# Kernel tuning notes

Measured on AMD Instinct MI355X. Metric: run time of the kernel, lower is better.

## Reference

```python
import jax, jax.numpy as jnp
import numpy as np

ALPHA = 0.2  # LeakyReLU negative slope
NEG_INF = -1e9


def setup_inputs() -> dict:
    key = jax.random.key(0)
    k1, k2, k3, k4 = jax.random.split(key, 4)
    B, N, IN, OUT = 8, 2048, 512, 32
    graph_input = jax.random.normal(k1, (B, N, IN), dtype=jnp.float32)
    adj = jax.random.randint(k2, (B, N, N), 0, 2, dtype=jnp.int32)
    W_fc = jax.random.normal(k3, (OUT, IN), dtype=jnp.float32) * (1.0 / np.sqrt(IN))
    W_attn = jax.random.normal(k4, (1, 2 * OUT), dtype=jnp.float32) * (1.0 / np.sqrt(2 * OUT))
    return {"graph_input": graph_input, "adj": adj, "W_fc": W_fc, "W_attn": W_attn}


def reference(graph_input, adj, W_fc, W_attn):
    # h: [B, N, 32]
    h = jnp.einsum('bni,oi->bno', graph_input, W_fc)
    out_dim = W_fc.shape[0]
    # attn_fc(cat(h_i, h_j)) is separable: a1.h_i + a2.h_j
    a1 = W_attn[0, :out_dim]   # [32]
    a2 = W_attn[0, out_dim:]   # [32]
    f1 = jnp.einsum('bno,o->bn', h, a1)  # [B, N]
    f2 = jnp.einsum('bno,o->bn', h, a2)  # [B, N]
    scores = jax.nn.leaky_relu(f1[:, :, None] + f2[:, None, :], negative_slope=ALPHA)  # [B,N,N]
    scores = jnp.where(adj == 0, NEG_INF, scores)
    attn = jax.nn.softmax(scores, axis=2)
    # NOTE: original multiplies attention with graph_input (not h)
    h_prime = jnp.einsum('bnm,bmi->bni', attn, graph_input)  # [B, N, IN]
    return jax.nn.elu(h_prime)  # concat=True path
```

## Files before the change

kernel.cpp:

```cpp
#include <hip/hip_runtime.h>
#include <hip/hip_bf16.h>

#define BATCH 8
#define NN    2048
#define FIN   512
#define FOUT  32
#define GALPHA 0.2f
#define NROW  128
#define NIT   32

typedef float  f32x4  __attribute__((ext_vector_type(4)));
typedef __bf16 bf16x8 __attribute__((ext_vector_type(8)));
typedef unsigned short u16;
typedef u16 u16x8 __attribute__((ext_vector_type(8)));

static __device__ __forceinline__ u16 f2bf(float f) {
    __hip_bfloat16 h = __float2bfloat16(f);
    union { __hip_bfloat16 h; u16 u; } c; c.h = h; return c.u;
}
static __device__ __forceinline__ float bf2f(u16 u) {
    union { u16 u; __hip_bfloat16 h; } c; c.u = u; return __bfloat162float(c.h);
}

__global__ __launch_bounds__(256) void k_prep(
    const float* __restrict__ x, const int* __restrict__ adj,
    const float* __restrict__ Wfc, const float* __restrict__ Wat,
    __hip_bfloat16* __restrict__ xt,
    float* __restrict__ f1, float* __restrict__ f2,
    unsigned int* __restrict__ bits)
{
    const int bx = blockIdx.x;
    const int it = bx & 7, mt = (bx >> 3) & 31, b = bx >> 8;
    const int m0 = mt * 64, i0 = it * 64;
    const int tt = threadIdx.x;

    __shared__ __align__(16) char smem[16384];
    u16 (*tile)[72]   = (u16(*)[72])smem;
    float* w1s        = (float*)(smem + 9216);
    float* w2s        = (float*)(smem + 9216 + 256);
    unsigned int* pls = (unsigned int*)smem;

    if (tt < 64) {
        const int i = i0 + tt;
        float s1 = 0.f, s2 = 0.f;
        #pragma unroll
        for (int o = 0; o < FOUT; o++) {
            float wv = Wfc[o * FIN + i];
            s1 += wv * Wat[o];
            s2 += wv * Wat[FOUT + o];
        }
        w1s[tt] = s1; w2s[tt] = s2;
    }
    __syncthreads();

    const int mm  = tt >> 3;
    const int icl = (tt & 7) * 8;
    const float* xb = x + ((size_t)b * NN + m0) * FIN + i0;
    f32x4 wA = *(const f32x4*)&w1s[icl];
    f32x4 wB = *(const f32x4*)&w1s[icl + 4];
    f32x4 wC = *(const f32x4*)&w2s[icl];
    f32x4 wD = *(const f32x4*)&w2s[icl + 4];
    float p1[2], p2[2];
    #pragma unroll
    for (int h = 0; h < 2; h++) {
        int m = mm + h * 32;
        const f32x4* src = (const f32x4*)(xb + (size_t)m * FIN + icl);
        f32x4 v0 = src[0], v1 = src[1];
        u16x8 pk;
        float s1 = 0.f, s2 = 0.f;
        #pragma unroll
        for (int j = 0; j < 4; j++) {
            pk[j] = f2bf(v0[j]); pk[4 + j] = f2bf(v1[j]);
            s1 += v0[j] * wA[j] + v1[j] * wB[j];
            s2 += v0[j] * wC[j] + v1[j] * wD[j];
        }
        p1[h] = s1; p2[h] = s2;
        *(u16x8*)&tile[m][icl] = pk;
    }
    #pragma unroll
    for (int off = 1; off < 8; off <<= 1) {
        p1[0] += __shfl_xor(p1[0], off); p1[1] += __shfl_xor(p1[1], off);
        p2[0] += __shfl_xor(p2[0], off); p2[1] += __shfl_xor(p2[1], off);
    }
    if ((tt & 7) == 0) {
        size_t r0 = (size_t)b * NN + m0 + mm;
        atomicAdd(&f1[r0], p1[0]);      atomicAdd(&f1[r0 + 32], p1[1]);
        atomicAdd(&f2[r0], p2[0]);      atomicAdd(&f2[r0 + 32], p2[1]);
    }
    __syncthreads();
    __hip_bfloat16* xtb = xt + ((size_t)b * FIN + i0) * NN + m0;
    const int mc = (tt & 7) * 8;
    #pragma unroll
    for (int h = 0; h < 2; h++) {
        int ii = (tt >> 3) + h * 32;
        u16x8 v;
        #pragma unroll
        for (int j = 0; j < 8; j++) v[j] = tile[mc + j][ii];
        *(u16x8*)(xtb + (size_t)ii * NN + mc) = v;
    }

    __syncthreads();
    {
        const int* ab = adj + (size_t)(b * NN + m0 + it * 8) * NN;
        #pragma unroll
        for (int s = 0; s < 16; s++) {
            int4 v = *(const int4*)(ab + (size_t)(s * 256 + tt) * 4);
            unsigned int pb = (v.x != 0 ? 0x00000001u : 0u)
                            | (v.y != 0 ? 0x00000100u : 0u)
                            | (v.z != 0 ? 0x00010000u : 0u)
                            | (v.w != 0 ? 0x01000000u : 0u);
            pls[s * 256 + tt] = pb;
        }
        __syncthreads();
        const int r = tt >> 5, c0 = tt & 31;
        #pragma unroll
        for (int half = 0; half < 2; half++) {
            const int c = c0 + half * 32;
            const unsigned int* q = pls + r * 512 + c * 8;
            unsigned int bv = 0;
            #pragma unroll
            for (int j = 0; j < 8; j++) {
                unsigned int pb = q[j];
                bv |= (pb         & 1u) << (j * 4 + 0);
                bv |= ((pb >> 8)  & 1u) << (j * 4 + 1);
                bv |= ((pb >> 16) & 1u) << (j * 4 + 2);
                bv |= ((pb >> 24) & 1u) << (j * 4 + 3);
            }
            bits[(size_t)(b * NN + m0 + it * 8 + r) * 64 + c] = bv;
        }
    }
}

__global__ __launch_bounds__(512, 2) void k_main(
    const unsigned int* __restrict__ bits, const __hip_bfloat16* __restrict__ xt,
    const float* __restrict__ f1, const float* __restrict__ f2,
    float* __restrict__ out)
{
    const int bx = blockIdx.x;
    const int b = bx & 7, rt = (bx >> 3) & 15, it = bx >> 7;
    const int n0 = rt * NROW;
    const int i0 = it * 256;
    const int tid = threadIdx.x;
    const int lane = tid & 63, wv = tid >> 6;
    const int quad = lane >> 4, l15 = lane & 15;

    __shared__ u16 At[2][NROW * 64];
    __shared__ float rs[NROW];

    const int grow = tid >> 2;
    const int q4   = tid & 3;
    const unsigned short* bp = (const unsigned short*)bits
                               + ((size_t)(b * NN) + n0 + grow) * 128 + q4;
    const float* f2p = f2 + b * NN + q4 * 16;
    const float  f1v = f1[b * NN + n0 + grow];
    const int swz = grow & 7;
    u16* wp0 = &At[0][grow * 64 + (((q4 * 2) ^ swz) * 8)];
    u16* wp1 = &At[0][grow * 64 + (((q4 * 2 + 1) ^ swz) * 8)];
    float rpart = 0.f;

    const __hip_bfloat16* xtp = xt + ((size_t)(b * FIN) + i0 + wv * 32 + l15) * NN + quad * 8;

    f32x4 acc[8][2];
    #pragma unroll
    for (int s = 0; s < 8; s++) { acc[s][0] = (f32x4){0,0,0,0}; acc[s][1] = (f32x4){0,0,0,0}; }

    auto gen = [&](int buf, unsigned int bv, const f32x4* fr) {
        u16x8 pk0, pk1;
        #pragma unroll
        for (int e = 0; e < 16; e++) {
            float s  = f1v + fr[e >> 2][e & 3];
            float ls = fmaxf(s, GALPHA * s);
            float ev = ((bv >> e) & 1u) ? __expf(ls) : 0.f;
            u16 hb = f2bf(ev);
            rpart += bf2f(hb);
            if (e < 8) pk0[e] = hb; else pk1[e - 8] = hb;
        }
        *(u16x8*)(wp0 + buf * (NROW * 64)) = pk0;
        *(u16x8*)(wp1 + buf * (NROW * 64)) = pk1;
    };

    {
        unsigned int b0 = bp[0];
        f32x4 g0[4];
        #pragma unroll
        for (int j = 0; j < 4; j++) g0[j] = *(const f32x4*)(f2p + j * 4);
        gen(0, b0, g0);
    }
    unsigned int brng[2];
    f32x4 frng[2][4];
    brng[1] = bp[4];
    #pragma unroll
    for (int j = 0; j < 4; j++) frng[1][j] = *(const f32x4*)(f2p + 64 + j * 4);
    brng[0] = bp[8];
    #pragma unroll
    for (int j = 0; j < 4; j++) frng[0][j] = *(const f32x4*)(f2p + 128 + j * 4);

    bf16x8 Bc[2][2], Bn[2][2];
    #pragma unroll
    for (int ks = 0; ks < 2; ks++)
        #pragma unroll
        for (int c = 0; c < 2; c++)
            Bc[ks][c] = *(const bf16x8*)(xtp + ks * 32 + (size_t)(c * 16) * NN);
    __syncthreads();

    #pragma unroll 2
    for (int t = 0; t < NIT; t++) {
        const int cur = t & 1;
        if (t < NIT - 1) {
            const __hip_bfloat16* xk = xtp + (t + 1) * 64;
            #pragma unroll
            for (int ks = 0; ks < 2; ks++)
                #pragma unroll
                for (int c = 0; c < 2; c++)
                    Bn[ks][c] = *(const bf16x8*)(xk + ks * 32 + (size_t)(c * 16) * NN);
        }
        #pragma unroll
        for (int ks = 0; ks < 2; ks++) {
            #pragma unroll
            for (int s = 0; s < 8; s++) {
                const int row = s * 16 + l15;
                bf16x8 Af = *(const bf16x8*)&At[cur][row * 64 + (((ks * 4 + quad) ^ (row & 7)) * 8)];
                acc[s][0] = __builtin_amdgcn_mfma_f32_16x16x32_bf16(Af, Bc[ks][0], acc[s][0], 0, 0, 0);
                acc[s][1] = __builtin_amdgcn_mfma_f32_16x16x32_bf16(Af, Bc[ks][1], acc[s][1], 0, 0, 0);
            }
        }
        if (t < NIT - 1) {
            gen(1 - cur, brng[(t + 1) & 1], frng[(t + 1) & 1]);
            if (t < NIT - 2) {
                brng[t & 1] = bp[(t + 2) * 4];
                #pragma unroll
                for (int j = 0; j < 4; j++)
                    frng[t & 1][j] = *(const f32x4*)(f2p + (t + 2) * 64 + j * 4);
            }
        }
        asm volatile("s_waitcnt lgkmcnt(0)\ns_barrier" ::: "memory");
        #pragma unroll
        for (int ks = 0; ks < 2; ks++) {
            Bc[ks][0] = Bn[ks][0]; Bc[ks][1] = Bn[ks][1];
        }
    }

    rpart += __shfl_xor(rpart, 1);
    rpart += __shfl_xor(rpart, 2);
    if (q4 == 0) rs[grow] = 1.0f / rpart;
    __syncthreads();

    #pragma unroll
    for (int s = 0; s < 8; s++) {
        #pragma unroll
        for (int r = 0; r < 4; r++) {
            const int row = s * 16 + quad * 4 + r;
            const float inv = rs[row];
            float* op = out + ((size_t)b * NN + (n0 + row)) * FIN + i0 + wv * 32 + l15;
            #pragma unroll
            for (int c = 0; c < 2; c++) {
                float v = acc[s][c][r] * inv;
                v = v > 0.f ? v : (__expf(v) - 1.f);
                op[c * 16] = v;
            }
        }
    }
}

extern "C" void kernel_launch(void* const* d_in, const int* in_sizes, int n_in,
                              void* d_out, int out_size, void* d_ws, size_t ws_size,
                              hipStream_t stream) {
    const float* x   = (const float*)d_in[0];
    const int*   adj = (const int*)d_in[1];
    const float* Wfc = (const float*)d_in[2];
    const float* Wat = (const float*)d_in[3];
    float* out = (float*)d_out;

    float* f1 = (float*)d_ws;
    float* f2 = f1 + BATCH * NN;
    unsigned int* bits = (unsigned int*)(f2 + BATCH * NN);
    __hip_bfloat16* xt = (__hip_bfloat16*)(bits + (size_t)BATCH * NN * 64);

    hipMemsetAsync(f1, 0, (size_t)2 * BATCH * NN * sizeof(float), stream);
    hipLaunchKernelGGL(k_prep, dim3(2048), dim3(256), 0, stream,
                       x, adj, Wfc, Wat, xt, f1, f2, bits);
    hipLaunchKernelGGL(k_main, dim3(256),  dim3(512), 0, stream,
                       bits, xt, f1, f2, out);
}
```

Measured before the change: 284.1 us.

## Fuse prep and main kernels into one cooperative launch with grid sync

Merges the preprocessing kernel (bf16 transpose of x, f1/f2 projection, adjacency bit-packing) and the attention-matmul kernel into a single cooperative kernel separated by a grid-wide barrier. Each prep block now owns a full 64-row strip across all 512 features, so f1/f2 are written directly instead of atomically accumulated, which removes the memset. This saves a launch and the memset but drops prep from 2048 blocks to 256 blocks looping serially. That may reduce memory-level parallelism in the bandwidth-bound adjacency read, and it adds grid-sync overhead.

```diff
diff --git a/kernel.cpp b/kernel.cpp
--- a/kernel.cpp
+++ b/kernel.cpp
@@ -1,5 +1,8 @@
 #include <hip/hip_runtime.h>
 #include <hip/hip_bf16.h>
+#include <hip/hip_cooperative_groups.h>
+
+namespace cg = cooperative_groups;
 
 #define BATCH 8
 #define NN    2048
@@ -22,241 +25,237 @@
     union { u16 u; __hip_bfloat16 h; } c; c.u = u; return __bfloat162float(c.h);
 }
 
-__global__ __launch_bounds__(256) void k_prep(
+__global__ __launch_bounds__(512, 2) void k_fused(
     const float* __restrict__ x, const int* __restrict__ adj,
     const float* __restrict__ Wfc, const float* __restrict__ Wat,
     __hip_bfloat16* __restrict__ xt,
     float* __restrict__ f1, float* __restrict__ f2,
-    unsigned int* __restrict__ bits)
-{
-    const int bx = blockIdx.x;
-    const int it = bx & 7, mt = (bx >> 3) & 31, b = bx >> 8;
-    const int m0 = mt * 64, i0 = it * 64;
-    const int tt = threadIdx.x;
-
-    __shared__ __align__(16) char smem[16384];
-    u16 (*tile)[72]   = (u16(*)[72])smem;
-    float* w1s        = (float*)(smem + 9216);
-    float* w2s        = (float*)(smem + 9216 + 256);
-    unsigned int* pls = (unsigned int*)smem;
-
-    if (tt < 64) {
-        const int i = i0 + tt;
-        float s1 = 0.f, s2 = 0.f;
-        #pragma unroll
-        for (int o = 0; o < FOUT; o++) {
-            float wv = Wfc[o * FIN + i];
-            s1 += wv * Wat[o];
-            s2 += wv * Wat[FOUT + o];
-        }
-        w1s[tt] = s1; w2s[tt] = s2;
-    }
-    __syncthreads();
-
-    const int mm  = tt >> 3;
-    const int icl = (tt & 7) * 8;
-    const float* xb = x + ((size_t)b * NN + m0) * FIN + i0;
-    f32x4 wA = *(const f32x4*)&w1s[icl];
-    f32x4 wB = *(const f32x4*)&w1s[icl + 4];
-    f32x4 wC = *(const f32x4*)&w2s[icl];
-    f32x4 wD = *(const f32x4*)&w2s[icl + 4];
-    float p1[2], p2[2];
-    #pragma unroll
-    for (int h = 0; h < 2; h++) {
-        int m = mm + h * 32;
-        const f32x4* src = (const f32x4*)(xb + (size_t)m * FIN + icl);
-        f32x4 v0 = src[0], v1 = src[1];
-        u16x8 pk;
-        float s1 = 0.f, s2 = 0.f;
-        #pragma unroll
-        for (int j = 0; j < 4; j++) {
-            pk[j] = f2bf(v0[j]); pk[4 + j] = f2bf(v1[j]);
-            s1 += v0[j] * wA[j] + v1[j] * wB[j];
-            s2 += v0[j] * wC[j] + v1[j] * wD[j];
-        }
-        p1[h] = s1; p2[h] = s2;
-        *(u16x8*)&tile[m][icl] = pk;
-    }
-    #pragma unroll
-    for (int off = 1; off < 8; off <<= 1) {
-        p1[0] += __shfl_xor(p1[0], off); p1[1] += __shfl_xor(p1[1], off);
-        p2[0] += __shfl_xor(p2[0], off); p2[1] += __shfl_xor(p2[1], off);
-    }
-    if ((tt & 7) == 0) {
-        size_t r0 = (size_t)b * NN + m0 + mm;
-        atomicAdd(&f1[r0], p1[0]);      atomicAdd(&f1[r0 + 32], p1[1]);
-        atomicAdd(&f2[r0], p2[0]);      atomicAdd(&f2[r0 + 32], p2[1]);
-    }
-    __syncthreads();
-    __hip_bfloat16* xtb = xt + ((size_t)b * FIN + i0) * NN + m0;
-    const int mc = (tt & 7) * 8;
-    #pragma unroll
-    for (int h = 0; h < 2; h++) {
-        int ii = (tt >> 3) + h * 32;
-        u16x8 v;
-        #pragma unroll
-        for (int j = 0; j < 8; j++) v[j] = tile[mc + j][ii];
-        *(u16x8*)(xtb + (size_t)ii * NN + mc) = v;
-    }
-
-    __syncthreads();
-    {
-        const int* ab = adj + (size_t)(b * NN + m0 + it * 8) * NN;
-        #pragma unroll
-        for (int s = 0; s < 16; s++) {
-            int4 v = *(const int4*)(ab + (size_t)(s * 256 + tt) * 4);
-            unsigned int pb = (v.x != 0 ? 0x00000001u : 0u)
-                            | (v.y != 0 ? 0x00000100u : 0u)
-                            | (v.z != 0 ? 0x00010000u : 0u)
-                            | (v.w != 0 ? 0x01000000u : 0u);
-            pls[s * 256 + tt] = pb;
-        }
-        __syncthreads();
-        const int r = tt >> 5, c0 = tt & 31;
-        #pragma unroll
-        for (int half = 0; half < 2; half++) {
-            const int c = c0 + half * 32;
-            const unsigned int* q = pls + r * 512 + c * 8;
-            unsigned int bv = 0;
-            #pragma unroll
-            for (int j = 0; j < 8; j++) {
-                unsigned int pb = q[j];
-                bv |= (pb         & 1u) << (j * 4 + 0);
-                bv |= ((pb >> 8)  & 1u) << (j * 4 + 1);
-                bv |= ((pb >> 16) & 1u) << (j * 4 + 2);
-                bv |= ((pb >> 24) & 1u) << (j * 4 + 3);
-            }
-            bits[(size_t)(b * NN + m0 + it * 8 + r) * 64 + c] = bv;
-        }
-    }
-}
-
-__global__ __launch_bounds__(512, 2) void k_main(
-    const unsigned int* __restrict__ bits, const __hip_bfloat16* __restrict__ xt,
-    const float* __restrict__ f1, const float* __restrict__ f2,
+    unsigned int* __restrict__ bits,
     float* __restrict__ out)
 {
-    const int bx = blockIdx.x;
-    const int b = bx & 7, rt = (bx >> 3) & 15, it = bx >> 7;
-    const int n0 = rt * NROW;
-    const int i0 = it * 256;
-    const int tid = threadIdx.x;
-    const int lane = tid & 63, wv = tid >> 6;
-    const int quad = lane >> 4, l15 = lane & 15;
-
-    __shared__ u16 At[2][NROW * 64];
-    __shared__ float rs[NROW];
-
-    const int grow = tid >> 2;
-    const int q4   = tid & 3;
-    const unsigned short* bp = (const unsigned short*)bits
-                               + ((size_t)(b * NN) + n0 + grow) * 128 + q4;
-    const float* f2p = f2 + b * NN + q4 * 16;
-    const float  f1v = f1[b * NN + n0 + grow];
-    const int swz = grow & 7;
-    u16* wp0 = &At[0][grow * 64 + (((q4 * 2) ^ swz) * 8)];
-    u16* wp1 = &At[0][grow * 64 + (((q4 * 2 + 1) ^ swz) * 8)];
-    float rpart = 0.f;
-
-    const __hip_bfloat16* xtp = xt + ((size_t)(b * FIN) + i0 + wv * 32 + l15) * NN + quad * 8;
-
-    f32x4 acc[8][2];
-    #pragma unroll
-    for (int s = 0; s < 8; s++) { acc[s][0] = (f32x4){0,0,0,0}; acc[s][1] = (f32x4){0,0,0,0}; }
-
-    auto gen = [&](int buf, unsigned int bv, const f32x4* fr) {
-        u16x8 pk0, pk1;
-        #pragma unroll
-        for (int e = 0; e < 16; e++) {
-            float s  = f1v + fr[e >> 2][e & 3];
-            float ls = fmaxf(s, GALPHA * s);
-            float ev = ((bv >> e) & 1u) ? __expf(ls) : 0.f;
-            u16 hb = f2bf(ev);
-            rpart += bf2f(hb);
-            if (e < 8) pk0[e] = hb; else pk1[e - 8] = hb;
-        }
-        *(u16x8*)(wp0 + buf * (NROW * 64)) = pk0;
-        *(u16x8*)(wp1 + buf * (NROW * 64)) = pk1;
-    };
+    __shared__ __align__(16) char smem[33280];
+    const int tt = threadIdx.x;
 
     {
-        unsigned int b0 = bp[0];
-        f32x4 g0[4];
-        #pragma unroll
-        for (int j = 0; j < 4; j++) g0[j] = *(const f32x4*)(f2p + j * 4);
-        gen(0, b0, g0);
+        const int b  = blockIdx.x >> 5;
+        const int mt = blockIdx.x & 31;
+        const int m0 = mt * 64;
+        u16 (*tile)[72]   = (u16(*)[72])smem;
+        float* w1s        = (float*)(smem + 9216);
+        float* w2s        = (float*)(smem + 11264);
+        unsigned int* pls = (unsigned int*)(smem + 13312);
+
+        {
+            float s1 = 0.f, s2 = 0.f;
+            #pragma unroll
+            for (int o = 0; o < FOUT; o++) {
+                float wv = Wfc[o * FIN + tt];
+                s1 += wv * Wat[o];
+                s2 += wv * Wat[FOUT + o];
+            }
+            w1s[tt] = s1; w2s[tt] = s2;
+        }
+        __syncthreads();
+
+        const int mm  = tt >> 3;
+        const int icl = (tt & 7) * 8;
+        float f1a = 0.f, f2a = 0.f;
+
+        for (int it = 0; it < 8; it++) {
+            const int i0 = it * 64;
+            const f32x4* src = (const f32x4*)(x + ((size_t)(b * NN + m0 + mm)) * FIN + i0 + icl);
+            f32x4 v0 = src[0], v1 = src[1];
+            f32x4 wA = *(const f32x4*)&w1s[i0 + icl];
+            f32x4 wB = *(const f32x4*)&w1s[i0 + icl + 4];
+            f32x4 wC = *(const f32x4*)&w2s[i0 + icl];
+            f32x4 wD = *(const f32x4*)&w2s[i0 + icl + 4];
+            u16x8 pk;
+            float s1 = 0.f, s2 = 0.f;
+            #pragma unroll
+            for (int j = 0; j < 4; j++) {
+                pk[j] = f2bf(v0[j]); pk[4 + j] = f2bf(v1[j]);
+                s1 += v0[j] * wA[j] + v1[j] * wB[j];
+                s2 += v0[j] * wC[j] + v1[j] * wD[j];
+            }
+            f1a += s1; f2a += s2;
+            *(u16x8*)&tile[mm][icl] = pk;
+            __syncthreads();
+            {
+                __hip_bfloat16* xtb = xt + ((size_t)b * FIN + i0) * NN + m0;
+                const int ii = tt >> 3;
+                const int mc = (tt & 7) * 8;
+                u16x8 v;
+                #pragma unroll
+                for (int j = 0; j < 8; j++) v[j] = tile[mc + j][ii];
+                *(u16x8*)(xtb + (size_t)ii * NN + mc) = v;
+            }
+            {
+                const int* ab = adj + (size_t)(b * NN + m0 + it * 8) * NN;
+                #pragma unroll
+                for (int s = 0; s < 8; s++) {
+                    int4 v = *(const int4*)(ab + (size_t)(s * 512 + tt) * 4);
+                    unsigned int pb = (v.x != 0 ? 0x00000001u : 0u)
+                                    | (v.y != 0 ? 0x00000100u : 0u)
+                                    | (v.z != 0 ? 0x00010000u : 0u)
+                                    | (v.w != 0 ? 0x01000000u : 0u);
+                    pls[s * 512 + tt] = pb;
+                }
+            }
+            __syncthreads();
+            {
+                const int r = tt >> 6, c = tt & 63;
+                const unsigned int* q = pls + r * 512 + c * 8;
+                unsigned int bv = 0;
+                #pragma unroll
+                for (int j = 0; j < 8; j++) {
+                    unsigned int pb = q[j];
+                    bv |= (pb         & 1u) << (j * 4 + 0);
+                    bv |= ((pb >> 8)  & 1u) << (j * 4 + 1);
+                    bv |= ((pb >> 16) & 1u) << (j * 4 + 2);
+                    bv |= ((pb >> 24) & 1u) << (j * 4 + 3);
+                }
+                bits[(size_t)(b * NN + m0 + it * 8 + r) * 64 + c] = bv;
+            }
+            if (it < 7) __syncthreads();
+        }
+        #pragma unroll
+        for (int off = 1; off < 8; off <<= 1) {
+            f1a += __shfl_xor(f1a, off);
+            f2a += __shfl_xor(f2a, off);
+        }
+        if ((tt & 7) == 0) {
+            f1[b * NN + m0 + mm] = f1a;
+            f2[b * NN + m0 + mm] = f2a;
+        }
     }
-    unsigned int brng[2];
-    f32x4 frng[2][4];
-    brng[1] = bp[4];
-    #pragma unroll
-    for (int j = 0; j < 4; j++) frng[1][j] = *(const f32x4*)(f2p + 64 + j * 4);
-    brng[0] = bp[8];
-    #pragma unroll
-    for (int j = 0; j < 4; j++) frng[0][j] = *(const f32x4*)(f2p + 128 + j * 4);
-
-    bf16x8 Bc[2][2], Bn[2][2];
-    #pragma unroll
-    for (int ks = 0; ks < 2; ks++)
-        #pragma unroll
-        for (int c = 0; c < 2; c++)
-            Bc[ks][c] = *(const bf16x8*)(xtp + ks * 32 + (size_t)(c * 16) * NN);
-    __syncthreads();
-
-    #pragma unroll 2
-    for (int t = 0; t < NIT; t++) {
-        const int cur = t & 1;
-        if (t < NIT - 1) {
-            const __hip_bfloat16* xk = xtp + (t + 1) * 64;
-            #pragma unroll
-            for (int ks = 0; ks < 2; ks++)
-                #pragma unroll
-                for (int c = 0; c < 2; c++)
-                    Bn[ks][c] = *(const bf16x8*)(xk + ks * 32 + (size_t)(c * 16) * NN);
-        }
-        #pragma unroll
-        for (int ks = 0; ks < 2; ks++) {
-            #pragma unroll
-            for (int s = 0; s < 8; s++) {
-                const int row = s * 16 + l15;
-                bf16x8 Af = *(const bf16x8*)&At[cur][row * 64 + (((ks * 4 + quad) ^ (row & 7)) * 8)];
-                acc[s][0] = __builtin_amdgcn_mfma_f32_16x16x32_bf16(Af, Bc[ks][0], acc[s][0], 0, 0, 0);
-                acc[s][1] = __builtin_amdgcn_mfma_f32_16x16x32_bf16(Af, Bc[ks][1], acc[s][1], 0, 0, 0);
-            }
-        }
-        if (t < NIT - 1) {
-            gen(1 - cur, brng[(t + 1) & 1], frng[(t + 1) & 1]);
-            if (t < NIT - 2) {
-                brng[t & 1] = bp[(t + 2) * 4];
-                #pragma unroll
-                for (int j = 0; j < 4; j++)
-                    frng[t & 1][j] = *(const f32x4*)(f2p + (t + 2) * 64 + j * 4);
-            }
-        }
-        asm volatile("s_waitcnt lgkmcnt(0)\ns_barrier" ::: "memory");
-        #pragma unroll
-        for (int ks = 0; ks < 2; ks++) {
-            Bc[ks][0] = Bn[ks][0]; Bc[ks][1] = Bn[ks][1];
-        }
-    }
-
-    rpart += __shfl_xor(rpart, 1);
-    rpart += __shfl_xor(rpart, 2);
-    if (q4 == 0) rs[grow] = 1.0f / rpart;
-    __syncthreads();
-
-    #pragma unroll
-    for (int s = 0; s < 8; s++) {
-        #pragma unroll
-        for (int r = 0; r < 4; r++) {
-            const int row = s * 16 + quad * 4 + r;
-            const float inv = rs[row];
-            float* op = out + ((size_t)b * NN + (n0 + row)) * FIN + i0 + wv * 32 + l15;
-            #pragma unroll
-            for (int c = 0; c < 2; c++) {
-                float v = acc[s][c][r] * inv;
-                v = v > 0.f ? v : (__expf(v) - 1.f);
-                op[c * 16] = v;
+
+    __threadfence();
+    cg::this_grid().sync();
+
+    {
+        const int bx = blockIdx.x;
+        const int b = bx & 7, rt = (bx >> 3) & 15, it = bx >> 7;
+        const int n0 = rt * NROW;
+        const int i0 = it * 256;
+        const int tid = tt;
+        const int lane = tid & 63, wv = tid >> 6;
+        const int quad = lane >> 4, l15 = lane & 15;
+
+        u16* Atb  = (u16*)smem;
+        float* rs = (float*)(smem + 32768);
+
+        const int grow = tid >> 2;
+        const int q4   = tid & 3;
+        const unsigned short* bp = (const unsigned short*)bits
+                                   + ((size_t)(b * NN) + n0 + grow) * 128 + q4;
+        const float* f2p = f2 + b * NN + q4 * 16;
+        const float  f1v = f1[b * NN + n0 + grow];
+        const int swz = grow & 7;
+        u16* wp0 = Atb + grow * 64 + (((q4 * 2) ^ swz) * 8);
+        u16* wp1 = Atb + grow * 64 + (((q4 * 2 + 1) ^ swz) * 8);
+        float rpart = 0.f;
+
+        const __hip_bfloat16* xtp = xt + ((size_t)(b * FIN) + i0 + wv * 32 + l15) * NN + quad * 8;
+
+        f32x4 acc[8][2];
+        #pragma unroll
+        for (int s = 0; s < 8; s++) { acc[s][0] = (f32x4){0,0,0,0}; acc[s][1] = (f32x4){0,0,0,0}; }
+
+        auto gen = [&](int buf, unsigned int bv, const f32x4* fr) {
+            u16x8 pk0, pk1;
+            #pragma unroll
+            for (int e = 0; e < 16; e++) {
+                float s  = f1v + fr[e >> 2][e & 3];
+                float ls = fmaxf(s, GALPHA * s);
+                float ev = ((bv >> e) & 1u) ? __expf(ls) : 0.f;
+                u16 hb = f2bf(ev);
+                rpart += bf2f(hb);
+                if (e < 8) pk0[e] = hb; else pk1[e - 8] = hb;
+            }
+            *(u16x8*)(wp0 + buf * (NROW * 64)) = pk0;
+            *(u16x8*)(wp1 + buf * (NROW * 64)) = pk1;
+        };
+
+        {
+            unsigned int b0 = bp[0];
+            f32x4 g0[4];
+            #pragma unroll
+            for (int j = 0; j < 4; j++) g0[j] = *(const f32x4*)(f2p + j * 4);
+            gen(0, b0, g0);
+        }
+        unsigned int brng[2];
+        f32x4 frng[2][4];
+        brng[1] = bp[4];
+        #pragma unroll
+        for (int j = 0; j < 4; j++) frng[1][j] = *(const f32x4*)(f2p + 64 + j * 4);
+        brng[0] = bp[8];
+        #pragma unroll
+        for (int j = 0; j < 4; j++) frng[0][j] = *(const f32x4*)(f2p + 128 + j * 4);
+
+        bf16x8 Bc[2][2], Bn[2][2];
+        #pragma unroll
+        for (int ks = 0; ks < 2; ks++)
+            #pragma unroll
+            for (int c = 0; c < 2; c++)
+                Bc[ks][c] = *(const bf16x8*)(xtp + ks * 32 + (size_t)(c * 16) * NN);
+        __syncthreads();
+
+        #pragma unroll 2
+        for (int t = 0; t < NIT; t++) {
+            const int cur = t & 1;
+            if (t < NIT - 1) {
+                const __hip_bfloat16* xk = xtp + (t + 1) * 64;
+                #pragma unroll
+                for (int ks = 0; ks < 2; ks++)
+                    #pragma unroll
+                    for (int c = 0; c < 2; c++)
+                        Bn[ks][c] = *(const bf16x8*)(xk + ks * 32 + (size_t)(c * 16) * NN);
+            }
+            #pragma unroll
+            for (int ks = 0; ks < 2; ks++) {
+                #pragma unroll
+                for (int s = 0; s < 8; s++) {
+                    const int row = s * 16 + l15;
+                    bf16x8 Af = *(const bf16x8*)(Atb + cur * (NROW * 64)
+                                  + row * 64 + (((ks * 4 + quad) ^ (row & 7)) * 8));
+                    acc[s][0] = __builtin_amdgcn_mfma_f32_16x16x32_bf16(Af, Bc[ks][0], acc[s][0], 0, 0, 0);
+                    acc[s][1] = __builtin_amdgcn_mfma_f32_16x16x32_bf16(Af, Bc[ks][1], acc[s][1], 0, 0, 0);
+                }
+            }
+            if (t < NIT - 1) {
+                gen(1 - cur, brng[(t + 1) & 1], frng[(t + 1) & 1]);
+                if (t < NIT - 2) {
+                    brng[t & 1] = bp[(t + 2) * 4];
+                    #pragma unroll
+                    for (int j = 0; j < 4; j++)
+                        frng[t & 1][j] = *(const f32x4*)(f2p + (t + 2) * 64 + j * 4);
+                }
+            }
+            asm volatile("s_waitcnt lgkmcnt(0)\ns_barrier" ::: "memory");
+            #pragma unroll
+            for (int ks = 0; ks < 2; ks++) {
+                Bc[ks][0] = Bn[ks][0]; Bc[ks][1] = Bn[ks][1];
+            }
+        }
+
+        rpart += __shfl_xor(rpart, 1);
+        rpart += __shfl_xor(rpart, 2);
+        if (q4 == 0) rs[grow] = 1.0f / rpart;
+        __syncthreads();
+
+        #pragma unroll
+        for (int s = 0; s < 8; s++) {
+            #pragma unroll
+            for (int r = 0; r < 4; r++) {
+                const int row = s * 16 + quad * 4 + r;
+                const float inv = rs[row];
+                float* op = out + ((size_t)b * NN + (n0 + row)) * FIN + i0 + wv * 32 + l15;
+                #pragma unroll
+                for (int c = 0; c < 2; c++) {
+                    float v = acc[s][c][r] * inv;
+                    v = v > 0.f ? v : (__expf(v) - 1.f);
+                    op[c * 16] = v;
+                }
             }
         }
     }
@@ -276,9 +275,8 @@
     unsigned int* bits = (unsigned int*)(f2 + BATCH * NN);
     __hip_bfloat16* xt = (__hip_bfloat16*)(bits + (size_t)BATCH * NN * 64);
 
-    hipMemsetAsync(f1, 0, (size_t)2 * BATCH * NN * sizeof(float), stream);
-    hipLaunchKernelGGL(k_prep, dim3(2048), dim3(256), 0, stream,
-                       x, adj, Wfc, Wat, xt, f1, f2, bits);
-    hipLaunchKernelGGL(k_main, dim3(256),  dim3(512), 0, stream,
-                       bits, xt, f1, f2, out);
-}
+    void* args[] = { (void*)&x, (void*)&adj, (void*)&Wfc, (void*)&Wat,
+                     (void*)&xt, (void*)&f1, (void*)&f2, (void*)&bits, (void*)&out };
+    hipLaunchCooperativeKernel((const void*)k_fused, dim3(256), dim3(512),
+                               args, 0, stream);
+}
```

Result: slower. 372.4 us (+31.1%).
